# Performance work log

Hardware: AMD Instinct MI355X
Metric: run time of the kernel (lower is better)

Reference implementation:

```python
import jax, jax.numpy as jnp
import numpy as np

B, T, D = 2, 2048, 1024
H, HD = 16, 64
DL, DC = 512, 256
THETA = 10000.0
LN_EPS = 1e-5


def setup_inputs() -> dict:
    key = jax.random.key(0)
    ks = jax.random.split(key, 8)
    s = 0.02
    return {
        "x": jax.random.normal(ks[0], (B, T, D), jnp.float32),
        "W_q": jax.random.normal(ks[1], (H * HD, D), jnp.float32) * s,
        "b_q": jnp.zeros((H * HD,), jnp.float32),
        "W_kvl": jax.random.normal(ks[2], (DL, D), jnp.float32) * s,
        "b_kvl": jnp.zeros((DL,), jnp.float32),
        "ts_scale": jnp.ones((DL,), jnp.float32),
        "ts_shift": jnp.zeros((DL,), jnp.float32),
        "W_comp": jax.random.normal(ks[3], (DC, DL), jnp.float32) * s,
        "W_exp": jax.random.normal(ks[4], (DL, DC), jnp.float32) * s,
        "ln_g": jnp.ones((DC,), jnp.float32),
        "ln_b": jnp.zeros((DC,), jnp.float32),
        "W_fkv": jax.random.normal(ks[5], (2 * H * HD, DL), jnp.float32) * s,
        "b_fkv": jnp.zeros((2 * H * HD,), jnp.float32),
        "W_out": jax.random.normal(ks[6], (D, H * HD), jnp.float32) * s,
        "b_out": jnp.zeros((D,), jnp.float32),
    }


def _rope_tables(t_len):
    inv_freq = 1.0 / (THETA ** (jnp.arange(0, HD, 2, dtype=jnp.float32) / HD))
    pos = jnp.arange(t_len, dtype=jnp.float32)
    freqs = pos[:, None] * inv_freq[None, :]          # [T, HD/2]
    cos = jnp.concatenate([jnp.cos(freqs)] * 2, -1)   # [T, HD]
    sin = jnp.concatenate([jnp.sin(freqs)] * 2, -1)
    return cos[None, None], sin[None, None]           # [1,1,T,HD]


def _rotate_half(z):
    return jnp.concatenate([-z[..., HD // 2:], z[..., :HD // 2]], -1)


def reference(x, W_q, b_q, W_kvl, b_kvl, ts_scale, ts_shift, W_comp, W_exp,
              ln_g, ln_b, W_fkv, b_fkv, W_out, b_out):
    # Q path: [B,T,D] -> [B,H,T,HD]
    q = (jnp.einsum('btd,ed->bte', x, W_q) + b_q).reshape(B, T, H, HD).transpose(0, 2, 1, 3)

    # KV latent + learned KVSplice bottleneck
    kvl = jnp.einsum('btd,ld->btl', x, W_kvl) + b_kvl                 # [B,T,DL]
    xt = kvl * jax.nn.softplus(ts_scale) + ts_shift
    c = jnp.einsum('btl,cl->btc', xt, W_comp)                         # [B,T,DC]
    mu = jnp.mean(c, -1, keepdims=True)
    var = jnp.mean(jnp.square(c - mu), -1, keepdims=True)
    c = (c - mu) * jax.lax.rsqrt(var + LN_EPS) * ln_g + ln_b
    dec = jnp.einsum('btc,lc->btl', c, W_exp)                         # [B,T,DL]

    # Decompress latent to K,V
    kv = jnp.einsum('btl,el->bte', dec, W_fkv) + b_fkv                # [B,T,2*H*HD]
    kv = kv.reshape(B, T, 2, H, HD).transpose(2, 0, 3, 1, 4)          # [2,B,H,T,HD]
    k, v = kv[0], kv[1]

    # RoPE
    cos, sin = _rope_tables(T)
    q = q * cos + _rotate_half(q) * sin
    k = k * cos + _rotate_half(k) * sin

    # Causal SDPA
    scale = 1.0 / np.sqrt(HD)
    scores = jnp.einsum('bhqd,bhkd->bhqk', q, k) * scale
    mask = jnp.tril(jnp.ones((T, T), bool))
    scores = jnp.where(mask, scores, jnp.float32(-1e30))
    attn = jax.nn.softmax(scores, axis=-1)
    o = jnp.einsum('bhqk,bhkd->bhqd', attn, v)
    o = o.transpose(0, 2, 1, 3).reshape(B, T, H * HD)
    return jnp.einsum('bte,de->btd', o, W_out) + b_out
```

## Files before the change

### kernel.cpp

```cpp
#include <hip/hip_runtime.h>
#include <math.h>

#define B_SZ   2
#define T_SEQ  2048
#define NH     16
#define HDIM   64
#define D_MOD  1024
#define DL     512
#define DC     256
#define MROWS  4096

typedef __attribute__((ext_vector_type(8))) short bf16x8;
typedef __attribute__((ext_vector_type(4))) float f32x4;

#define SCALE_Q 0.18033688011112042f

static __device__ __forceinline__ unsigned short f2bf(float f) {
    union { float f; unsigned u; } v; v.f = f;
    unsigned r = v.u + 0x7fffu + ((v.u >> 16) & 1u);
    return (unsigned short)(r >> 16);
}

static __device__ __forceinline__ void gl_lds16(const unsigned short* g,
                                                unsigned short* l) {
    __builtin_amdgcn_global_load_lds(
        (const __attribute__((address_space(1))) unsigned int*)g,
        (__attribute__((address_space(3))) unsigned int*)l, 16, 0, 0);
}

__global__ __launch_bounds__(256) void cvt_bf16(
    const float* __restrict__ x,  const float* __restrict__ wq,
    const float* __restrict__ wkvl, const float* __restrict__ wcomp,
    const float* __restrict__ wexp, const float* __restrict__ wfkv,
    const float* __restrict__ wout,
    unsigned short* __restrict__ xb,  unsigned short* __restrict__ wqh,
    unsigned short* __restrict__ wkvlh, unsigned short* __restrict__ wcomph,
    unsigned short* __restrict__ wexph, unsigned short* __restrict__ wfkvh,
    unsigned short* __restrict__ wouth, float2* __restrict__ rope_tab)
{
    const int g = blockIdx.x * 256 + threadIdx.x;
    const int stride = gridDim.x * 256;
#define CVT_SEG(src, dst, n4)                                              \
    for (int i = g; i < (n4); i += stride) {                               \
        float4 v = ((const float4*)(src))[i];                              \
        unsigned short h[4] = {f2bf(v.x), f2bf(v.y), f2bf(v.z), f2bf(v.w)};\
        *(uint2*)((dst) + (size_t)i * 4) = *(uint2*)h;                     \
    }
    CVT_SEG(x, xb, 1048576)
    CVT_SEG(wq, wqh, 262144)
    CVT_SEG(wkvl, wkvlh, 131072)
    CVT_SEG(wcomp, wcomph, 32768)
    CVT_SEG(wexp, wexph, 32768)
    CVT_SEG(wfkv, wfkvh, 262144)
    CVT_SEG(wout, wouth, 262144)
#undef CVT_SEG
    for (int i = g; i < T_SEQ * 32; i += stride) {
        const int t = i >> 5, fi = i & 31;
        const float inv = __expf((float)fi * (-9.210340371976184f / 32.0f));
        float sn, cs; sincosf((float)t * inv, &sn, &cs);
        rope_tab[i] = make_float2(cs, sn);
    }
}

#define GEMM64x128_PROLOG(Aptr, Wptr, Kdim)                                    \
    __shared__ unsigned short As[64 * 32];                                     \
    __shared__ unsigned short Ws[128 * 32];                                    \
    const int tid = threadIdx.x;                                               \
    const int w = tid >> 6, lane = tid & 63;                                   \
    const int l16 = lane & 15, quad = lane >> 4;                               \
    const int wm = w >> 1, wn = w & 1;                                         \
    const int srow = lane >> 2, scol = (lane & 3) << 3;                        \
    const unsigned short* Ag = (Aptr) + (size_t)(m0 + w * 16 + srow) * (Kdim) + scol; \
    const unsigned short* Wg = (Wptr) + (size_t)(n0 + w * 32 + srow) * (Kdim) + scol; \
    unsigned short* Al  = &As[w * 512];                                        \
    unsigned short* Wl0 = &Ws[w * 1024];                                       \
    unsigned short* Wl1 = &Ws[w * 1024 + 512];                                 \
    f32x4 acc[2][4];                                                           \
    _Pragma("unroll") for (int i = 0; i < 2; ++i)                              \
        _Pragma("unroll") for (int j = 0; j < 4; ++j)                          \
            acc[i][j] = (f32x4){0.f, 0.f, 0.f, 0.f};                           \
    for (int k0 = 0; k0 < (Kdim); k0 += 32) {                                  \
        __syncthreads();                                                       \
        gl_lds16(Ag + k0, Al);                                                 \
        gl_lds16(Wg + k0, Wl0);                                                \
        gl_lds16(Wg + (size_t)16 * (Kdim) + k0, Wl1);                          \
        __syncthreads();                                                       \
        bf16x8 af[2], bfr[4];                                                  \
        _Pragma("unroll") for (int i = 0; i < 2; ++i)                          \
            af[i] = *(const bf16x8*)&As[(wm * 32 + i * 16 + l16) * 32 + quad * 8]; \
        _Pragma("unroll") for (int j = 0; j < 4; ++j)                          \
            bfr[j] = *(const bf16x8*)&Ws[(wn * 64 + j * 16 + l16) * 32 + quad * 8]; \
        _Pragma("unroll") for (int i = 0; i < 2; ++i)                          \
            _Pragma("unroll") for (int j = 0; j < 4; ++j)                      \
                acc[i][j] = __builtin_amdgcn_mfma_f32_16x16x32_bf16(           \
                    af[i], bfr[j], acc[i][j], 0, 0, 0);                        \
    }

__global__ __launch_bounds__(256) void gemm_qxt(
    const unsigned short* __restrict__ A, const unsigned short* __restrict__ Wq,
    const unsigned short* __restrict__ Wkvl,
    const float* __restrict__ b_q, const float* __restrict__ b_kvl,
    const float* __restrict__ ts_scale, const float* __restrict__ ts_shift,
    const float2* __restrict__ tab,
    unsigned short* __restrict__ qh, unsigned short* __restrict__ xt)
{
    const int m0 = blockIdx.x * 64;
    const bool is_q = (blockIdx.y < 8);
    const int n0 = is_q ? blockIdx.y * 128 : (blockIdx.y - 8) * 128;
    const unsigned short* W = is_q ? Wq : Wkvl;

    GEMM64x128_PROLOG(A, W, D_MOD)

    if (is_q) {
#pragma unroll
        for (int i = 0; i < 2; ++i) {
#pragma unroll
            for (int j = 0; j < 4; ++j) {
                const int col = n0 + wn * 64 + j * 16 + l16;
                const int h = col >> 6, hd = col & 63;
                const float bv = b_q[col];
                const float bvp = b_q[col ^ 32];
                const float sgn = (hd < 32) ? -1.f : 1.f;
#pragma unroll
                for (int reg = 0; reg < 4; ++reg) {
                    const int row = m0 + wm * 32 + i * 16 + quad * 4 + reg;
                    const int b = row >> 11, t = row & (T_SEQ - 1);
                    const float2 cssn = tab[t * 32 + (hd & 31)];
                    const float v  = acc[i][j][reg] + bv;
                    const float vp = acc[i][j ^ 2][reg] + bvp;
                    const float r = (v * cssn.x + sgn * vp * cssn.y) * SCALE_Q;
                    qh[(((size_t)b * NH + h) * T_SEQ + t) * HDIM + hd] = f2bf(r);
                }
            }
        }
    } else {
#pragma unroll
        for (int i = 0; i < 2; ++i) {
#pragma unroll
            for (int j = 0; j < 4; ++j) {
                const int col = n0 + wn * 64 + j * 16 + l16;
                const float bv = b_kvl[col];
                const float sp_s = log1pf(expf(ts_scale[col]));
                const float sp_t = ts_shift[col];
#pragma unroll
                for (int reg = 0; reg < 4; ++reg) {
                    const int row = m0 + wm * 32 + i * 16 + quad * 4 + reg;
                    const float val = (acc[i][j][reg] + bv) * sp_s + sp_t;
                    xt[(size_t)row * DL + col] = f2bf(val);
                }
            }
        }
    }
}

__global__ __launch_bounds__(256) void gemm_kv(
    const unsigned short* __restrict__ A, const unsigned short* __restrict__ W,
    const float* __restrict__ bias, const float2* __restrict__ tab,
    unsigned short* __restrict__ kh, unsigned short* __restrict__ vth)
{
    const int m0 = blockIdx.x * 64, n0 = blockIdx.y * 128;

    GEMM64x128_PROLOG(A, W, DL)

    if (n0 < 1024) {
#pragma unroll
        for (int i = 0; i < 2; ++i) {
#pragma unroll
            for (int j = 0; j < 4; ++j) {
                const int col = n0 + wn * 64 + j * 16 + l16;
                const int h = (col >> 6) & 15, hd = col & 63;
                const float bv = bias[col];
                const float bvp = bias[col ^ 32];
                const float sgn = (hd < 32) ? -1.f : 1.f;
#pragma unroll
                for (int reg = 0; reg < 4; ++reg) {
                    const int row = m0 + wm * 32 + i * 16 + quad * 4 + reg;
                    const int b = row >> 11, t = row & (T_SEQ - 1);
                    const float2 cssn = tab[t * 32 + (hd & 31)];
                    const float v  = acc[i][j][reg] + bv;
                    const float vp = acc[i][j ^ 2][reg] + bvp;
                    const float r = v * cssn.x + sgn * vp * cssn.y;
                    kh[(((size_t)b * NH + h) * T_SEQ + t) * HDIM + hd] = f2bf(r);
                }
            }
        }
    } else {
#pragma unroll
        for (int i = 0; i < 2; ++i) {
#pragma unroll
            for (int j = 0; j < 4; ++j) {
                const int col = n0 + wn * 64 + j * 16 + l16;
                const int cv = col - 1024;
                const int h = cv >> 6, hd = cv & 63;
                const float bv = bias[col];
                unsigned short hv[4];
                const int r0 = m0 + wm * 32 + i * 16 + quad * 4;
                const int b = r0 >> 11, t0 = r0 & (T_SEQ - 1);
#pragma unroll
                for (int reg = 0; reg < 4; ++reg)
                    hv[reg] = f2bf(acc[i][j][reg] + bv);
                *(uint2*)&vth[(((size_t)b * NH + h) * HDIM + hd) * T_SEQ + t0] =
                    *(uint2*)hv;
            }
        }
    }
}

__global__ __launch_bounds__(256) void gemm_out(
    const unsigned short* __restrict__ A, const unsigned short* __restrict__ W,
    const float* __restrict__ bias, float* __restrict__ C)
{
    const int m0 = blockIdx.x * 64, n0 = blockIdx.y * 128;

    GEMM64x128_PROLOG(A, W, D_MOD)

#pragma unroll
    for (int i = 0; i < 2; ++i)
#pragma unroll
        for (int j = 0; j < 4; ++j) {
            const int col = n0 + wn * 64 + j * 16 + l16;
            const float bv = bias[col];
#pragma unroll
            for (int reg = 0; reg < 4; ++reg) {
                const int row = m0 + wm * 32 + i * 16 + quad * 4 + reg;
                C[(size_t)row * D_MOD + col] = acc[i][j][reg] + bv;
            }
        }
}

__global__ __launch_bounds__(256) void gemm_c_ln(
    const unsigned short* __restrict__ A, const unsigned short* __restrict__ W,
    const float* __restrict__ g, const float* __restrict__ bta,
    unsigned short* __restrict__ outb)
{
    __shared__ unsigned short As[16 * 32];
    __shared__ unsigned short Ws[256 * 32];
    __shared__ float redS[4][16];
    __shared__ float redQ[4][16];

    const int tid = threadIdx.x;
    const int w = tid >> 6, lane = tid & 63;
    const int l16 = lane & 15, quad = lane >> 4;
    const int m0 = blockIdx.x * 16;

    const int srow = lane >> 2, scol = (lane & 3) << 3;
    const unsigned short* Ag = A + (size_t)(m0 + srow) * DL + scol;
    const unsigned short* Wg = W + (size_t)(w * 64 + srow) * DL + scol;

    f32x4 acc[4];
#pragma unroll
    for (int j = 0; j < 4; ++j) acc[j] = (f32x4){0.f, 0.f, 0.f, 0.f};

    for (int k0 = 0; k0 < DL; k0 += 32) {
        __syncthreads();
        if (w == 0) gl_lds16(Ag + k0, &As[0]);
#pragma unroll
        for (int c = 0; c < 4; ++c)
            gl_lds16(Wg + (size_t)(c * 16) * DL + k0, &Ws[(w * 64 + c * 16) * 32]);
        __syncthreads();

        const bf16x8 af = *(const bf16x8*)&As[l16 * 32 + quad * 8];
        bf16x8 bfr[4];
#pragma unroll
        for (int j = 0; j < 4; ++j)
            bfr[j] = *(const bf16x8*)&Ws[(w * 64 + j * 16 + l16) * 32 + quad * 8];
#pragma unroll
        for (int j = 0; j < 4; ++j)
            acc[j] = __builtin_amdgcn_mfma_f32_16x16x32_bf16(af, bfr[j], acc[j], 0, 0, 0);
    }

    float s[4], q2[4];
#pragma unroll
    for (int reg = 0; reg < 4; ++reg) {
        float sv = (acc[0][reg] + acc[1][reg]) + (acc[2][reg] + acc[3][reg]);
        float qv = (acc[0][reg] * acc[0][reg] + acc[1][reg] * acc[1][reg]) +
                   (acc[2][reg] * acc[2][reg] + acc[3][reg] * acc[3][reg]);
#pragma unroll
        for (int off = 1; off < 16; off <<= 1) {
            sv += __shfl_xor(sv, off);
            qv += __shfl_xor(qv, off);
        }
        s[reg] = sv; q2[reg] = qv;
    }
    if (l16 == 0) {
#pragma unroll
        for (int reg = 0; reg < 4; ++reg) {
            redS[w][quad * 4 + reg] = s[reg];
            redQ[w][quad * 4 + reg] = q2[reg];
        }
    }
    __syncthreads();

#pragma unroll
    for (int reg = 0; reg < 4; ++reg) {
        const int r = quad * 4 + reg;
        const float sum = (redS[0][r] + redS[1][r]) + (redS[2][r] + redS[3][r]);
        const float sq  = (redQ[0][r] + redQ[1][r]) + (redQ[2][r] + redQ[3][r]);
        const float mu  = sum * (1.0f / DC);
        const float var = sq * (1.0f / DC) - mu * mu;
        const float rstd = rsqrtf(var + 1e-5f);
#pragma unroll
        for (int j = 0; j < 4; ++j) {
            const int col = w * 64 + j * 16 + l16;
            const float val = (acc[j][reg] - mu) * rstd * g[col] + bta[col];
            outb[(size_t)(m0 + r) * DC + col] = f2bf(val);
        }
    }
}

__global__ __launch_bounds__(256) void gemm_mfma64_b(
    const unsigned short* __restrict__ A, const unsigned short* __restrict__ W,
    unsigned short* __restrict__ Cv, int N, int K)
{
    __shared__ unsigned short As[64 * 32];
    __shared__ unsigned short Ws[64 * 32];

    const int tid = threadIdx.x;
    const int w = tid >> 6, lane = tid & 63;
    const int l16 = lane & 15, quad = lane >> 4;
    const int wm = w >> 1, wn = w & 1;
    const int m0 = blockIdx.x * 64, n0 = blockIdx.y * 64;

    const unsigned short* Ag = A + (size_t)(m0 + w * 16 + (lane >> 2)) * K + ((lane & 3) << 3);
    const unsigned short* Wg = W + (size_t)(n0 + w * 16 + (lane >> 2)) * K + ((lane & 3) << 3);
    unsigned short* Al = &As[w * 512];
    unsigned short* Wl = &Ws[w * 512];

    f32x4 acc[2][2];
#pragma unroll
    for (int i = 0; i < 2; ++i)
#pragma unroll
        for (int j = 0; j < 2; ++j) acc[i][j] = (f32x4){0.f, 0.f, 0.f, 0.f};

    for (int k0 = 0; k0 < K; k0 += 32) {
        __syncthreads();
        gl_lds16(Ag + k0, Al);
        gl_lds16(Wg + k0, Wl);
        __syncthreads();

        bf16x8 af[2], bfr[2];
#pragma unroll
        for (int i = 0; i < 2; ++i)
            af[i] = *(const bf16x8*)&As[(wm * 32 + i * 16 + l16) * 32 + quad * 8];
#pragma unroll
        for (int j = 0; j < 2; ++j)
            bfr[j] = *(const bf16x8*)&Ws[(wn * 32 + j * 16 + l16) * 32 + quad * 8];
#pragma unroll
        for (int i = 0; i < 2; ++i)
#pragma unroll
            for (int j = 0; j < 2; ++j)
                acc[i][j] = __builtin_amdgcn_mfma_f32_16x16x32_bf16(
                    af[i], bfr[j], acc[i][j], 0, 0, 0);
    }

#pragma unroll
    for (int i = 0; i < 2; ++i) {
#pragma unroll
        for (int j = 0; j < 2; ++j) {
            const int col = n0 + wn * 32 + j * 16 + l16;
#pragma unroll
            for (int reg = 0; reg < 4; ++reg) {
                const int row = m0 + wm * 32 + i * 16 + quad * 4 + reg;
                Cv[(size_t)row * N + col] = f2bf(acc[i][j][reg]);
            }
        }
    }
}

__global__ __launch_bounds__(256, 3) void flash_mfma(
    const unsigned short* __restrict__ q, const unsigned short* __restrict__ k,
    const unsigned short* __restrict__ vt, unsigned short* __restrict__ o)
{
    __shared__ unsigned short Ks[64 * 72];
    __shared__ unsigned short Vs[64 * 72];
    __shared__ unsigned short Ps[128 * 72];

    const int bh = blockIdx.x & 31;
    const int j  = 15 - (blockIdx.x >> 5);
    const int q0 = j * 128;
    const int tid = threadIdx.x;
    const int w = tid >> 6, lane = tid & 63;
    const int l16 = lane & 15, quad = lane >> 4;

    bf16x8 qf[2][2];
#pragma unroll
    for (int mt = 0; mt < 2; ++mt)
#pragma unroll
        for (int kk = 0; kk < 2; ++kk)
            qf[mt][kk] = *(const bf16x8*)(q +
                ((size_t)bh * T_SEQ + q0 + w * 32 + mt * 16 + l16) * HDIM + kk * 32 + quad * 8);

    f32x4 of[2][4];
    float lrow[2][4];
#pragma unroll
    for (int mt = 0; mt < 2; ++mt) {
#pragma unroll
        for (int dt = 0; dt < 4; ++dt) of[mt][dt] = (f32x4){0.f, 0.f, 0.f, 0.f};
#pragma unroll
        for (int r = 0; r < 4; ++r) lrow[mt][r] = 0.f;
    }

    const int ldr = tid >> 2;
    const int ldc = (tid & 3) * 16;
    const unsigned short* kgb = k + ((size_t)bh * T_SEQ + ldr) * HDIM + ldc;
    const unsigned short* vgb = vt + ((size_t)bh * HDIM + ldr) * T_SEQ + ldc;

    const int kend = q0 + 128;
    for (int k0 = 0; k0 < kend; k0 += 64) {
        __syncthreads();
        {
            const unsigned short* kg = kgb + (size_t)k0 * HDIM;
            *(bf16x8*)&Ks[ldr * 72 + ldc]     = *(const bf16x8*)kg;
            *(bf16x8*)&Ks[ldr * 72 + ldc + 8] = *(const bf16x8*)(kg + 8);
            const unsigned short* vg = vgb + k0;
            *(bf16x8*)&Vs[ldr * 72 + ldc]     = *(const bf16x8*)vg;
            *(bf16x8*)&Vs[ldr * 72 + ldc + 8] = *(const bf16x8*)(vg + 8);
        }
        __syncthreads();

        bf16x8 kf[4][2];
#pragma unroll
        for (int nt = 0; nt < 4; ++nt)
#pragma unroll
            for (int kk = 0; kk < 2; ++kk)
                kf[nt][kk] = *(const bf16x8*)&Ks[(nt * 16 + l16) * 72 + kk * 32 + quad * 8];

#pragma unroll
        for (int mt = 0; mt < 2; ++mt) {
            const int rbase = q0 + w * 32 + mt * 16;
            f32x4 sf[4];
#pragma unroll
            for (int nt = 0; nt < 4; ++nt) {
                sf[nt] = (f32x4){0.f, 0.f, 0.f, 0.f};
#pragma unroll
                for (int kk = 0; kk < 2; ++kk)
                    sf[nt] = __builtin_amdgcn_mfma_f32_16x16x32_bf16(qf[mt][kk], kf[nt][kk], sf[nt], 0, 0, 0);
            }
            const bool need_mask = (k0 + 63) > rbase;
#pragma unroll
            for (int reg = 0; reg < 4; ++reg) {
                float a0 = sf[0][reg], a1 = sf[1][reg], a2 = sf[2][reg], a3 = sf[3][reg];
                if (need_mask) {
                    const int tq = rbase + quad * 4 + reg;
                    if (k0 +      l16 > tq) a0 = -1e30f;
                    if (k0 + 16 + l16 > tq) a1 = -1e30f;
                    if (k0 + 32 + l16 > tq) a2 = -1e30f;
                    if (k0 + 48 + l16 > tq) a3 = -1e30f;
                }
                union { float f; unsigned u; } u0, u1, u2, u3;
                u0.f = exp2f(a0); u1.f = exp2f(a1);
                u2.f = exp2f(a2); u3.f = exp2f(a3);
                const int prow = (w * 32 + mt * 16 + quad * 4 + reg) * 72 + l16;
                Ps[prow]      = (unsigned short)(u0.u >> 16);
                Ps[prow + 16] = (unsigned short)(u1.u >> 16);
                Ps[prow + 32] = (unsigned short)(u2.u >> 16);
                Ps[prow + 48] = (unsigned short)(u3.u >> 16);
                u0.u &= 0xffff0000u; u1.u &= 0xffff0000u;
                u2.u &= 0xffff0000u; u3.u &= 0xffff0000u;
                lrow[mt][reg] += (u0.f + u1.f) + (u2.f + u3.f);
            }
        }

        bf16x8 vf[4][2];
#pragma unroll
        for (int dt = 0; dt < 4; ++dt)
#pragma unroll
            for (int kk = 0; kk < 2; ++kk)
                vf[dt][kk] = *(const bf16x8*)&Vs[(dt * 16 + l16) * 72 + kk * 32 + quad * 8];

#pragma unroll
        for (int mt = 0; mt < 2; ++mt) {
            bf16x8 pf[2];
#pragma unroll
            for (int kk = 0; kk < 2; ++kk)
                pf[kk] = *(const bf16x8*)&Ps[(w * 32 + mt * 16 + l16) * 72 + kk * 32 + quad * 8];
#pragma unroll
            for (int dt = 0; dt < 4; ++dt)
#pragma unroll
                for (int kk = 0; kk < 2; ++kk)
                    of[mt][dt] = __builtin_amdgcn_mfma_f32_16x16x32_bf16(pf[kk], vf[dt][kk], of[mt][dt], 0, 0, 0);
        }
    }

    const int b = bh >> 4, h = bh & 15;
#pragma unroll
    for (int mt = 0; mt < 2; ++mt) {
        const int rbase = q0 + w * 32 + mt * 16;
#pragma unroll
        for (int reg = 0; reg < 4; ++reg) {
            float l = lrow[mt][reg];
            l += __shfl_xor(l, 1);
            l += __shfl_xor(l, 2);
            l += __shfl_xor(l, 4);
            l += __shfl_xor(l, 8);
            const float inv = 1.0f / l;
            const int t = rbase + quad * 4 + reg;
#pragma unroll
            for (int dt = 0; dt < 4; ++dt)
                o[((size_t)b * T_SEQ + t) * (NH * HDIM) + h * HDIM + dt * 16 + l16] =
                    f2bf(of[mt][dt][reg] * inv);
        }
    }
}

extern "C" void kernel_launch(void* const* d_in, const int* in_sizes, int n_in,
                              void* d_out, int out_size, void* d_ws, size_t ws_size,
                              hipStream_t stream)
{
    (void)in_sizes; (void)n_in; (void)out_size; (void)ws_size;

    const float* x        = (const float*)d_in[0];
    const float* W_q      = (const float*)d_in[1];
    const float* b_q      = (const float*)d_in[2];
    const float* W_kvl    = (const float*)d_in[3];
    const float* b_kvl    = (const float*)d_in[4];
    const float* ts_scale = (const float*)d_in[5];
    const float* ts_shift = (const float*)d_in[6];
    const float* W_comp   = (const float*)d_in[7];
    const float* W_exp    = (const float*)d_in[8];
    const float* ln_g     = (const float*)d_in[9];
    const float* ln_b     = (const float*)d_in[10];
    const float* W_fkv    = (const float*)d_in[11];
    const float* b_fkv    = (const float*)d_in[12];
    const float* W_out    = (const float*)d_in[13];
    const float* b_out    = (const float*)d_in[14];
    float* out = (float*)d_out;

    char* p = (char*)d_ws;
    unsigned short* xb     = (unsigned short*)p;             p += 8  * 1024 * 1024;
    unsigned short* wqh    = (unsigned short*)p;             p += 2  * 1024 * 1024;
    unsigned short* wkvlh  = (unsigned short*)p;             p += 1  * 1024 * 1024;
    unsigned short* wcomph = (unsigned short*)p;             p += 256 * 1024;
    unsigned short* wexph  = (unsigned short*)p;             p += 256 * 1024;
    unsigned short* wfkvh  = (unsigned short*)p;             p += 2  * 1024 * 1024;
    unsigned short* wouth  = (unsigned short*)p;             p += 2  * 1024 * 1024;
    unsigned short* qh     = (unsigned short*)p;             p += 8  * 1024 * 1024;
    unsigned short* kh     = (unsigned short*)p;             p += 8  * 1024 * 1024;
    unsigned short* vth    = (unsigned short*)p;             p += 8  * 1024 * 1024;
    unsigned short* xt     = (unsigned short*)p;             p += 4  * 1024 * 1024;
    unsigned short* cbh    = (unsigned short*)p;             p += 2  * 1024 * 1024;
    unsigned short* dec    = (unsigned short*)p;             p += 4  * 1024 * 1024;
    unsigned short* ob     = (unsigned short*)p;             p += 8  * 1024 * 1024;
    float2*         tab    = (float2*)p;                     p += 512 * 1024;

    const dim3 blk(256);

    cvt_bf16<<<1024, blk, 0, stream>>>(x, W_q, W_kvl, W_comp, W_exp, W_fkv, W_out,
                                       xb, wqh, wkvlh, wcomph, wexph, wfkvh, wouth,
                                       tab);

    gemm_qxt<<<dim3(64, 12), blk, 0, stream>>>(
        xb, wqh, wkvlh, b_q, b_kvl, ts_scale, ts_shift, tab, qh, xt);

    gemm_c_ln<<<256, blk, 0, stream>>>(
        xt, wcomph, ln_g, ln_b, cbh);

    gemm_mfma64_b<<<dim3(64, 8), blk, 0, stream>>>(
        cbh, wexph, dec, DL, DC);

    gemm_kv<<<dim3(64, 16), blk, 0, stream>>>(
        dec, wfkvh, b_fkv, tab, kh, vth);

    flash_mfma<<<512, blk, 0, stream>>>(qh, kh, vth, ob);

    gemm_out<<<dim3(64, 8), blk, 0, stream>>>(
        ob, wouth, b_out, out);
}
```

Baseline: 248.3 us.

## Halve GEMM and flash-attention tile sizes to double block counts

```diff
diff --git a/kernel.cpp b/kernel.cpp
--- a/kernel.cpp
+++ b/kernel.cpp
@@ -62,38 +62,31 @@
     }
 }
 
-#define GEMM64x128_PROLOG(Aptr, Wptr, Kdim)                                    \
+#define GEMM64R_PROLOG(Aptr, Wptr, Kdim)                                       \
     __shared__ unsigned short As[64 * 32];                                     \
-    __shared__ unsigned short Ws[128 * 32];                                    \
+    __shared__ unsigned short Ws[64 * 32];                                     \
     const int tid = threadIdx.x;                                               \
     const int w = tid >> 6, lane = tid & 63;                                   \
     const int l16 = lane & 15, quad = lane >> 4;                               \
-    const int wm = w >> 1, wn = w & 1;                                         \
     const int srow = lane >> 2, scol = (lane & 3) << 3;                        \
     const unsigned short* Ag = (Aptr) + (size_t)(m0 + w * 16 + srow) * (Kdim) + scol; \
-    const unsigned short* Wg = (Wptr) + (size_t)(n0 + w * 32 + srow) * (Kdim) + scol; \
-    unsigned short* Al  = &As[w * 512];                                        \
-    unsigned short* Wl0 = &Ws[w * 1024];                                       \
-    unsigned short* Wl1 = &Ws[w * 1024 + 512];                                 \
-    f32x4 acc[2][4];                                                           \
-    _Pragma("unroll") for (int i = 0; i < 2; ++i)                              \
-        _Pragma("unroll") for (int j = 0; j < 4; ++j)                          \
-            acc[i][j] = (f32x4){0.f, 0.f, 0.f, 0.f};                           \
+    const unsigned short* Wg = (Wptr) + (size_t)(n0 + w * 16 + srow) * (Kdim) + scol; \
+    unsigned short* Al = &As[w * 512];                                         \
+    unsigned short* Wl = &Ws[w * 512];                                         \
+    f32x4 acc[4];                                                              \
+    _Pragma("unroll") for (int j = 0; j < 4; ++j)                              \
+        acc[j] = (f32x4){0.f, 0.f, 0.f, 0.f};                                  \
     for (int k0 = 0; k0 < (Kdim); k0 += 32) {                                  \
         __syncthreads();                                                       \
         gl_lds16(Ag + k0, Al);                                                 \
-        gl_lds16(Wg + k0, Wl0);                                                \
-        gl_lds16(Wg + (size_t)16 * (Kdim) + k0, Wl1);                          \
+        gl_lds16(Wg + k0, Wl);                                                 \
         __syncthreads();                                                       \
-        bf16x8 af[2], bfr[4];                                                  \
-        _Pragma("unroll") for (int i = 0; i < 2; ++i)                          \
-            af[i] = *(const bf16x8*)&As[(wm * 32 + i * 16 + l16) * 32 + quad * 8]; \
+        const bf16x8 af = *(const bf16x8*)&As[(w * 16 + l16) * 32 + quad * 8]; \
+        bf16x8 bfr[4];                                                         \
         _Pragma("unroll") for (int j = 0; j < 4; ++j)                          \
-            bfr[j] = *(const bf16x8*)&Ws[(wn * 64 + j * 16 + l16) * 32 + quad * 8]; \
-        _Pragma("unroll") for (int i = 0; i < 2; ++i)                          \
-            _Pragma("unroll") for (int j = 0; j < 4; ++j)                      \
-                acc[i][j] = __builtin_amdgcn_mfma_f32_16x16x32_bf16(           \
-                    af[i], bfr[j], acc[i][j], 0, 0, 0);                        \
+            bfr[j] = *(const bf16x8*)&Ws[(j * 16 + l16) * 32 + quad * 8];      \
+        _Pragma("unroll") for (int j = 0; j < 4; ++j)                          \
+            acc[j] = __builtin_amdgcn_mfma_f32_16x16x32_bf16(af, bfr[j], acc[j], 0, 0, 0); \
     }
 
 __global__ __launch_bounds__(256) void gemm_qxt(
@@ -105,49 +98,43 @@
     unsigned short* __restrict__ qh, unsigned short* __restrict__ xt)
 {
     const int m0 = blockIdx.x * 64;
-    const bool is_q = (blockIdx.y < 8);
-    const int n0 = is_q ? blockIdx.y * 128 : (blockIdx.y - 8) * 128;
+    const bool is_q = (blockIdx.y < 16);
+    const int n0 = is_q ? blockIdx.y * 64 : (blockIdx.y - 16) * 64;
     const unsigned short* W = is_q ? Wq : Wkvl;
 
-    GEMM64x128_PROLOG(A, W, D_MOD)
+    GEMM64R_PROLOG(A, W, D_MOD)
 
     if (is_q) {
 #pragma unroll
-        for (int i = 0; i < 2; ++i) {
-#pragma unroll
-            for (int j = 0; j < 4; ++j) {
-                const int col = n0 + wn * 64 + j * 16 + l16;
-                const int h = col >> 6, hd = col & 63;
-                const float bv = b_q[col];
-                const float bvp = b_q[col ^ 32];
-                const float sgn = (hd < 32) ? -1.f : 1.f;
-#pragma unroll
-                for (int reg = 0; reg < 4; ++reg) {
-                    const int row = m0 + wm * 32 + i * 16 + quad * 4 + reg;
-                    const int b = row >> 11, t = row & (T_SEQ - 1);
-                    const float2 cssn = tab[t * 32 + (hd & 31)];
-                    const float v  = acc[i][j][reg] + bv;
-                    const float vp = acc[i][j ^ 2][reg] + bvp;
-                    const float r = (v * cssn.x + sgn * vp * cssn.y) * SCALE_Q;
-                    qh[(((size_t)b * NH + h) * T_SEQ + t) * HDIM + hd] = f2bf(r);
-                }
+        for (int j = 0; j < 4; ++j) {
+            const int col = n0 + j * 16 + l16;
+            const int h = col >> 6, hd = col & 63;
+            const float bv = b_q[col];
+            const float bvp = b_q[col ^ 32];
+            const float sgn = (hd < 32) ? -1.f : 1.f;
+#pragma unroll
+            for (int reg = 0; reg < 4; ++reg) {
+                const int row = m0 + w * 16 + quad * 4 + reg;
+                const int b = row >> 11, t = row & (T_SEQ - 1);
+                const float2 cssn = tab[t * 32 + (hd & 31)];
+                const float v  = acc[j][reg] + bv;
+                const float vp = acc[j ^ 2][reg] + bvp;
+                const float r = (v * cssn.x + sgn * vp * cssn.y) * SCALE_Q;
+                qh[(((size_t)b * NH + h) * T_SEQ + t) * HDIM + hd] = f2bf(r);
             }
         }
     } else {
 #pragma unroll
-        for (int i = 0; i < 2; ++i) {
-#pragma unroll
-            for (int j = 0; j < 4; ++j) {
-                const int col = n0 + wn * 64 + j * 16 + l16;
-                const float bv = b_kvl[col];
-                const float sp_s = log1pf(expf(ts_scale[col]));
-                const float sp_t = ts_shift[col];
-#pragma unroll
-                for (int reg = 0; reg < 4; ++reg) {
-                    const int row = m0 + wm * 32 + i * 16 + quad * 4 + reg;
-                    const float val = (acc[i][j][reg] + bv) * sp_s + sp_t;
-                    xt[(size_t)row * DL + col] = f2bf(val);
-                }
+        for (int j = 0; j < 4; ++j) {
+            const int col = n0 + j * 16 + l16;
+            const float bv = b_kvl[col];
+            const float sp_s = log1pf(expf(ts_scale[col]));
+            const float sp_t = ts_shift[col];
+#pragma unroll
+            for (int reg = 0; reg < 4; ++reg) {
+                const int row = m0 + w * 16 + quad * 4 + reg;
+                const float val = (acc[j][reg] + bv) * sp_s + sp_t;
+                xt[(size_t)row * DL + col] = f2bf(val);
             }
         }
     }
@@ -158,50 +145,44 @@
     const float* __restrict__ bias, const float2* __restrict__ tab,
     unsigned short* __restrict__ kh, unsigned short* __restrict__ vth)
 {
-    const int m0 = blockIdx.x * 64, n0 = blockIdx.y * 128;
-
-    GEMM64x128_PROLOG(A, W, DL)
+    const int m0 = blockIdx.x * 64, n0 = blockIdx.y * 64;
+
+    GEMM64R_PROLOG(A, W, DL)
 
     if (n0 < 1024) {
 #pragma unroll
-        for (int i = 0; i < 2; ++i) {
-#pragma unroll
-            for (int j = 0; j < 4; ++j) {
-                const int col = n0 + wn * 64 + j * 16 + l16;
-                const int h = (col >> 6) & 15, hd = col & 63;
-                const float bv = bias[col];
-                const float bvp = bias[col ^ 32];
-                const float sgn = (hd < 32) ? -1.f : 1.f;
-#pragma unroll
-                for (int reg = 0; reg < 4; ++reg) {
-                    const int row = m0 + wm * 32 + i * 16 + quad * 4 + reg;
-                    const int b = row >> 11, t = row & (T_SEQ - 1);
-                    const float2 cssn = tab[t * 32 + (hd & 31)];
-                    const float v  = acc[i][j][reg] + bv;
-                    const float vp = acc[i][j ^ 2][reg] + bvp;
-                    const float r = v * cssn.x + sgn * vp * cssn.y;
-                    kh[(((size_t)b * NH + h) * T_SEQ + t) * HDIM + hd] = f2bf(r);
-                }
+        for (int j = 0; j < 4; ++j) {
+            const int col = n0 + j * 16 + l16;
+            const int h = (col >> 6) & 15, hd = col & 63;
+            const float bv = bias[col];
+            const float bvp = bias[col ^ 32];
+            const float sgn = (hd < 32) ? -1.f : 1.f;
+#pragma unroll
+            for (int reg = 0; reg < 4; ++reg) {
+                const int row = m0 + w * 16 + quad * 4 + reg;
+                const int b = row >> 11, t = row & (T_SEQ - 1);
+                const float2 cssn = tab[t * 32 + (hd & 31)];
+                const float v  = acc[j][reg] + bv;
+                const float vp = acc[j ^ 2][reg] + bvp;
+                const float r = v * cssn.x + sgn * vp * cssn.y;
+                kh[(((size_t)b * NH + h) * T_SEQ + t) * HDIM + hd] = f2bf(r);
             }
         }
     } else {
 #pragma unroll
-        for (int i = 0; i < 2; ++i) {
-#pragma unroll
-            for (int j = 0; j < 4; ++j) {
-                const int col = n0 + wn * 64 + j * 16 + l16;
-                const int cv = col - 1024;
-                const int h = cv >> 6, hd = cv & 63;
-                const float bv = bias[col];
-                unsigned short hv[4];
-                const int r0 = m0 + wm * 32 + i * 16 + quad * 4;
-                const int b = r0 >> 11, t0 = r0 & (T_SEQ - 1);
-#pragma unroll
-                for (int reg = 0; reg < 4; ++reg)
-                    hv[reg] = f2bf(acc[i][j][reg] + bv);
-                *(uint2*)&vth[(((size_t)b * NH + h) * HDIM + hd) * T_SEQ + t0] =
-                    *(uint2*)hv;
-            }
+        for (int j = 0; j < 4; ++j) {
+            const int col = n0 + j * 16 + l16;
+            const int cv = col - 1024;
+            const int h = cv >> 6, hd = cv & 63;
+            const float bv = bias[col];
+            unsigned short hv[4];
+            const int r0 = m0 + w * 16 + quad * 4;
+            const int b = r0 >> 11, t0 = r0 & (T_SEQ - 1);
+#pragma unroll
+            for (int reg = 0; reg < 4; ++reg)
+                hv[reg] = f2bf(acc[j][reg] + bv);
+            *(uint2*)&vth[(((size_t)b * NH + h) * HDIM + hd) * T_SEQ + t0] =
+                *(uint2*)hv;
         }
     }
 }
@@ -210,22 +191,20 @@
     const unsigned short* __restrict__ A, const unsigned short* __restrict__ W,
     const float* __restrict__ bias, float* __restrict__ C)
 {
-    const int m0 = blockIdx.x * 64, n0 = blockIdx.y * 128;
-
-    GEMM64x128_PROLOG(A, W, D_MOD)
-
-#pragma unroll
-    for (int i = 0; i < 2; ++i)
-#pragma unroll
-        for (int j = 0; j < 4; ++j) {
-            const int col = n0 + wn * 64 + j * 16 + l16;
-            const float bv = bias[col];
-#pragma unroll
-            for (int reg = 0; reg < 4; ++reg) {
-                const int row = m0 + wm * 32 + i * 16 + quad * 4 + reg;
-                C[(size_t)row * D_MOD + col] = acc[i][j][reg] + bv;
-            }
-        }
+    const int m0 = blockIdx.x * 64, n0 = blockIdx.y * 64;
+
+    GEMM64R_PROLOG(A, W, D_MOD)
+
+#pragma unroll
+    for (int j = 0; j < 4; ++j) {
+        const int col = n0 + j * 16 + l16;
+        const float bv = bias[col];
+#pragma unroll
+        for (int reg = 0; reg < 4; ++reg) {
+            const int row = m0 + w * 16 + quad * 4 + reg;
+            C[(size_t)row * D_MOD + col] = acc[j][reg] + bv;
+        }
+    }
 }
 
 __global__ __launch_bounds__(256) void gemm_c_ln(
@@ -373,39 +352,34 @@
 {
     __shared__ unsigned short Ks[64 * 72];
     __shared__ unsigned short Vs[64 * 72];
-    __shared__ unsigned short Ps[128 * 72];
+    __shared__ unsigned short Ps[64 * 72];
 
     const int bh = blockIdx.x & 31;
-    const int j  = 15 - (blockIdx.x >> 5);
-    const int q0 = j * 128;
+    const int j  = 31 - (blockIdx.x >> 5);
+    const int q0 = j * 64;
     const int tid = threadIdx.x;
     const int w = tid >> 6, lane = tid & 63;
     const int l16 = lane & 15, quad = lane >> 4;
-
-    bf16x8 qf[2][2];
-#pragma unroll
-    for (int mt = 0; mt < 2; ++mt)
-#pragma unroll
-        for (int kk = 0; kk < 2; ++kk)
-            qf[mt][kk] = *(const bf16x8*)(q +
-                ((size_t)bh * T_SEQ + q0 + w * 32 + mt * 16 + l16) * HDIM + kk * 32 + quad * 8);
-
-    f32x4 of[2][4];
-    float lrow[2][4];
-#pragma unroll
-    for (int mt = 0; mt < 2; ++mt) {
-#pragma unroll
-        for (int dt = 0; dt < 4; ++dt) of[mt][dt] = (f32x4){0.f, 0.f, 0.f, 0.f};
-#pragma unroll
-        for (int r = 0; r < 4; ++r) lrow[mt][r] = 0.f;
-    }
+    const int rbase = q0 + w * 16;
+
+    bf16x8 qf[2];
+#pragma unroll
+    for (int kk = 0; kk < 2; ++kk)
+        qf[kk] = *(const bf16x8*)(q + ((size_t)bh * T_SEQ + rbase + l16) * HDIM + kk * 32 + quad * 8);
+
+    f32x4 of[4];
+    float lrow[4];
+#pragma unroll
+    for (int dt = 0; dt < 4; ++dt) of[dt] = (f32x4){0.f, 0.f, 0.f, 0.f};
+#pragma unroll
+    for (int r = 0; r < 4; ++r) lrow[r] = 0.f;
 
     const int ldr = tid >> 2;
     const int ldc = (tid & 3) * 16;
     const unsigned short* kgb = k + ((size_t)bh * T_SEQ + ldr) * HDIM + ldc;
     const unsigned short* vgb = vt + ((size_t)bh * HDIM + ldr) * T_SEQ + ldc;
 
-    const int kend = q0 + 128;
+    const int kend = (j + 1) * 64;
     for (int k0 = 0; k0 < kend; k0 += 64) {
         __syncthreads();
         {
@@ -425,40 +399,37 @@
             for (int kk = 0; kk < 2; ++kk)
                 kf[nt][kk] = *(const bf16x8*)&Ks[(nt * 16 + l16) * 72 + kk * 32 + quad * 8];
 
-#pragma unroll
-        for (int mt = 0; mt < 2; ++mt) {
-            const int rbase = q0 + w * 32 + mt * 16;
-            f32x4 sf[4];
-#pragma unroll
-            for (int nt = 0; nt < 4; ++nt) {
-                sf[nt] = (f32x4){0.f, 0.f, 0.f, 0.f};
-#pragma unroll
-                for (int kk = 0; kk < 2; ++kk)
-                    sf[nt] = __builtin_amdgcn_mfma_f32_16x16x32_bf16(qf[mt][kk], kf[nt][kk], sf[nt], 0, 0, 0);
+        f32x4 sf[4];
+#pragma unroll
+        for (int nt = 0; nt < 4; ++nt) {
+            sf[nt] = (f32x4){0.f, 0.f, 0.f, 0.f};
+#pragma unroll
+            for (int kk = 0; kk < 2; ++kk)
+                sf[nt] = __builtin_amdgcn_mfma_f32_16x16x32_bf16(qf[kk], kf[nt][kk], sf[nt], 0, 0, 0);
+        }
+
+        const bool need_mask = (k0 + 63) > rbase;
+#pragma unroll
+        for (int reg = 0; reg < 4; ++reg) {
+            float a0 = sf[0][reg], a1 = sf[1][reg], a2 = sf[2][reg], a3 = sf[3][reg];
+            if (need_mask) {
+                const int tq = rbase + quad * 4 + reg;
+                if (k0 +      l16 > tq) a0 = -1e30f;
+                if (k0 + 16 + l16 > tq) a1 = -1e30f;
+                if (k0 + 32 + l16 > tq) a2 = -1e30f;
+                if (k0 + 48 + l16 > tq) a3 = -1e30f;
             }
-            const bool need_mask = (k0 + 63) > rbase;
-#pragma unroll
-            for (int reg = 0; reg < 4; ++reg) {
-                float a0 = sf[0][reg], a1 = sf[1][reg], a2 = sf[2][reg], a3 = sf[3][reg];
-                if (need_mask) {
-                    const int tq = rbase + quad * 4 + reg;
-                    if (k0 +      l16 > tq) a0 = -1e30f;
-                    if (k0 + 16 + l16 > tq) a1 = -1e30f;
-                    if (k0 + 32 + l16 > tq) a2 = -1e30f;
-                    if (k0 + 48 + l16 > tq) a3 = -1e30f;
-                }
-                union { float f; unsigned u; } u0, u1, u2, u3;
-                u0.f = exp2f(a0); u1.f = exp2f(a1);
-                u2.f = exp2f(a2); u3.f = exp2f(a3);
-                const int prow = (w * 32 + mt * 16 + quad * 4 + reg) * 72 + l16;
-                Ps[prow]      = (unsigned short)(u0.u >> 16);
-                Ps[prow + 16] = (unsigned short)(u1.u >> 16);
-                Ps[prow + 32] = (unsigned short)(u2.u >> 16);
-                Ps[prow + 48] = (unsigned short)(u3.u >> 16);
-                u0.u &= 0xffff0000u; u1.u &= 0xffff0000u;
-                u2.u &= 0xffff0000u; u3.u &= 0xffff0000u;
-                lrow[mt][reg] += (u0.f + u1.f) + (u2.f + u3.f);
-            }
+            union { float f; unsigned u; } u0, u1, u2, u3;
+            u0.f = exp2f(a0); u1.f = exp2f(a1);
+            u2.f = exp2f(a2); u3.f = exp2f(a3);
+            const int prow = (w * 16 + quad * 4 + reg) * 72 + l16;
+            Ps[prow]      = (unsigned short)(u0.u >> 16);
+            Ps[prow + 16] = (unsigned short)(u1.u >> 16);
+            Ps[prow + 32] = (unsigned short)(u2.u >> 16);
+            Ps[prow + 48] = (unsigned short)(u3.u >> 16);
+            u0.u &= 0xffff0000u; u1.u &= 0xffff0000u;
+            u2.u &= 0xffff0000u; u3.u &= 0xffff0000u;
+            lrow[reg] += (u0.f + u1.f) + (u2.f + u3.f);
         }
 
         bf16x8 vf[4][2];
@@ -468,38 +439,31 @@
             for (int kk = 0; kk < 2; ++kk)
                 vf[dt][kk] = *(const bf16x8*)&Vs[(dt * 16 + l16) * 72 + kk * 32 + quad * 8];
 
-#pragma unroll
-        for (int mt = 0; mt < 2; ++mt) {
-            bf16x8 pf[2];
+        bf16x8 pf[2];
+#pragma unroll
+        for (int kk = 0; kk < 2; ++kk)
+            pf[kk] = *(const bf16x8*)&Ps[(w * 16 + l16) * 72 + kk * 32 + quad * 8];
+#pragma unroll
+        for (int dt = 0; dt < 4; ++dt)
 #pragma unroll
             for (int kk = 0; kk < 2; ++kk)
-                pf[kk] = *(const bf16x8*)&Ps[(w * 32 + mt * 16 + l16) * 72 + kk * 32 + quad * 8];
-#pragma unroll
-            for (int dt = 0; dt < 4; ++dt)
-#pragma unroll
-                for (int kk = 0; kk < 2; ++kk)
-                    of[mt][dt] = __builtin_amdgcn_mfma_f32_16x16x32_bf16(pf[kk], vf[dt][kk], of[mt][dt], 0, 0, 0);
-        }
+                of[dt] = __builtin_amdgcn_mfma_f32_16x16x32_bf16(pf[kk], vf[dt][kk], of[dt], 0, 0, 0);
     }
 
     const int b = bh >> 4, h = bh & 15;
 #pragma unroll
-    for (int mt = 0; mt < 2; ++mt) {
-        const int rbase = q0 + w * 32 + mt * 16;
-#pragma unroll
-        for (int reg = 0; reg < 4; ++reg) {
-            float l = lrow[mt][reg];
-            l += __shfl_xor(l, 1);
-            l += __shfl_xor(l, 2);
-            l += __shfl_xor(l, 4);
-            l += __shfl_xor(l, 8);
-            const float inv = 1.0f / l;
-            const int t = rbase + quad * 4 + reg;
-#pragma unroll
-            for (int dt = 0; dt < 4; ++dt)
-                o[((size_t)b * T_SEQ + t) * (NH * HDIM) + h * HDIM + dt * 16 + l16] =
-                    f2bf(of[mt][dt][reg] * inv);
-        }
+    for (int reg = 0; reg < 4; ++reg) {
+        float l = lrow[reg];
+        l += __shfl_xor(l, 1);
+        l += __shfl_xor(l, 2);
+        l += __shfl_xor(l, 4);
+        l += __shfl_xor(l, 8);
+        const float inv = 1.0f / l;
+        const int t = rbase + quad * 4 + reg;
+#pragma unroll
+        for (int dt = 0; dt < 4; ++dt)
+            o[((size_t)b * T_SEQ + t) * (NH * HDIM) + h * HDIM + dt * 16 + l16] =
+                f2bf(of[dt][reg] * inv);
     }
 }
 
@@ -549,7 +513,7 @@
                                        xb, wqh, wkvlh, wcomph, wexph, wfkvh, wouth,
                                        tab);
 
-    gemm_qxt<<<dim3(64, 12), blk, 0, stream>>>(
+    gemm_qxt<<<dim3(64, 24), blk, 0, stream>>>(
         xb, wqh, wkvlh, b_q, b_kvl, ts_scale, ts_shift, tab, qh, xt);
 
     gemm_c_ln<<<256, blk, 0, stream>>>(
@@ -558,11 +522,11 @@
     gemm_mfma64_b<<<dim3(64, 8), blk, 0, stream>>>(
         cbh, wexph, dec, DL, DC);
 
-    gemm_kv<<<dim3(64, 16), blk, 0, stream>>>(
+    gemm_kv<<<dim3(64, 32), blk, 0, stream>>>(
         dec, wfkvh, b_fkv, tab, kh, vth);
 
-    flash_mfma<<<512, blk, 0, stream>>>(qh, kh, vth, ob);
-
-    gemm_out<<<dim3(64, 8), blk, 0, stream>>>(
+    flash_mfma<<<1024, blk, 0, stream>>>(qh, kh, vth, ob);
+
+    gemm_out<<<dim3(64, 16), blk, 0, stream>>>(
         ob, wouth, b_out, out);
 }
```

After: 240.9 us. 1.03x faster.
